# Kernel tuning notes

Hardware: AMD Instinct MI355X
Metric: run time of the kernel (lower is better)

Reference implementation:

```python
import jax, jax.numpy as jnp
import numpy as np

H = 8          # heads
V = 25         # num_nodes
C_IN = 64      # node_channel_in
C_OUT = 64     # node_channel_out
D_IN = V * C_IN    # 1600
D_OUT = V * C_OUT  # 1600


def setup_inputs() -> dict:
    key = jax.random.key(0)
    ks = jax.random.split(key, 7)
    s = 1.0 / np.sqrt(D_IN)  # torch Linear default init scale (uniform bound)
    x = jax.random.normal(ks[0], (16, C_IN, 512, V), dtype=jnp.float32)
    Wq = jax.random.uniform(ks[1], (H, D_IN, D_OUT), jnp.float32, -s, s)
    Wk = jax.random.uniform(ks[2], (H, D_IN, D_OUT), jnp.float32, -s, s)
    Wv = jax.random.uniform(ks[3], (H, D_IN, D_OUT), jnp.float32, -s, s)
    bq = jax.random.uniform(ks[4], (H, D_OUT), jnp.float32, -s, s)
    bk = jax.random.uniform(ks[5], (H, D_OUT), jnp.float32, -s, s)
    bv = jax.random.uniform(ks[6], (H, D_OUT), jnp.float32, -s, s)
    return {"x": x, "Wq": Wq, "bq": bq, "Wk": Wk, "bk": bk, "Wv": Wv, "bv": bv}


def reference(x, Wq, bq, Wk, bk, Wv, bv):
    n, c, t, v = x.shape
    # (n, c, t, v) -> (n, t, c*v)
    xf = jnp.transpose(x, (0, 2, 1, 3)).reshape(n, t, c * v)
    # fused per-head projections: batched GEMM over head axis
    q = jnp.einsum('ntd,hde->nhte', xf, Wq) + bq[None, :, None, :]
    k = jnp.einsum('ntd,hde->nhte', xf, Wk) + bk[None, :, None, :]
    val = jnp.einsum('ntd,hde->nhte', xf, Wv) + bv[None, :, None, :]
    scale = 1.0 / np.sqrt(C_OUT * V).astype(np.float32)
    att = jnp.einsum('nhte,nhse->nhts', q, k) * scale  # [n,h,t,t]
    att = jax.nn.softmax(att, axis=-1)
    o = jnp.einsum('nhts,nhse->nhte', att, val)  # [n,h,t,d_out]
    # (n,h,t,d) -> (n,t,d,h) -> (n,t,v,c_out*h) -> (n,c_out*h,t,v)
    o = jnp.transpose(o, (0, 2, 3, 1)).reshape(n, t, V, C_OUT * H)
    return jnp.transpose(o, (0, 3, 1, 2))
```

## Files before the change

### kernel.cpp

```cpp
#include <hip/hip_runtime.h>
#include <stdint.h>

#define NB    16
#define H8    8
#define T512  512
#define D1600 1600
#define EP    1664

typedef short s16x8 __attribute__((ext_vector_type(8)));
typedef float f32x4 __attribute__((ext_vector_type(4)));

__device__ __forceinline__ unsigned short f2bf(float f) {
  unsigned int u = __builtin_bit_cast(unsigned int, f);
  u += 0x7FFFu + ((u >> 16) & 1u);
  return (unsigned short)(u >> 16);
}

__device__ __forceinline__ void gld_lds16(const void* g, void* l) {
  __builtin_amdgcn_global_load_lds(
      (const __attribute__((address_space(1))) unsigned int*)g,
      (__attribute__((address_space(3))) unsigned int*)l, 16, 0, 0);
}

__global__ __launch_bounds__(256)
void conv_x_k(const float* __restrict__ x, unsigned short* __restrict__ xf) {
  size_t i = (size_t)blockIdx.x * 256 + threadIdx.x;
  if (i >= (size_t)NB * T512 * D1600) return;
  int d  = (int)(i % D1600);
  size_t nt = i / D1600;
  int t  = (int)(nt % T512);
  int n  = (int)(nt / T512);
  int c = d / 25, v = d % 25;
  xf[i] = f2bf(x[(((size_t)n * 64 + c) * 512 + t) * 25 + v]);
}

__global__ __launch_bounds__(256)
void conv_w_k(const float* __restrict__ Wq, const float* __restrict__ Wk,
              const float* __restrict__ Wv, unsigned short* __restrict__ Wt) {
  __shared__ float tile[32][33];
  int b = blockIdx.z, i3 = b >> 3, h = b & 7;
  const float* W = (i3 == 0 ? Wq : i3 == 1 ? Wk : Wv) + (size_t)h * D1600 * D1600;
  unsigned short* Wo = Wt + (size_t)b * EP * D1600;
  int e0 = blockIdx.x * 32, d0 = blockIdx.y * 32;
  int tx = threadIdx.x & 31, ty = threadIdx.x >> 5;
#pragma unroll
  for (int j = 0; j < 4; ++j) {
    int d = d0 + ty + j * 8, e = e0 + tx;
    tile[ty + j * 8][tx] = (e < D1600) ? W[(size_t)d * D1600 + e] : 0.f;
  }
  __syncthreads();
#pragma unroll
  for (int j = 0; j < 4; ++j) {
    int e = e0 + ty + j * 8, d = d0 + tx;
    Wo[(size_t)e * D1600 + d] = f2bf(tile[tx][ty + j * 8]);
  }
}

template <int MODE>
__global__ __launch_bounds__(256, 2)
void gemm_nt(const unsigned short* __restrict__ Ag,
             const unsigned short* __restrict__ Bg,
             float* __restrict__ Cf,
             unsigned short* __restrict__ Qo, unsigned short* __restrict__ Ko,
             unsigned short* __restrict__ Vo,
             const float* __restrict__ bq, const float* __restrict__ bk,
             const float* __restrict__ bv,
             int Klen, int lda, int ldb, float scale, int zbase) {
  constexpr int BM = 128, BN = 128, BK = 64;
  __shared__ unsigned short As[BM * BK];
  __shared__ unsigned short Bs[BN * BK];

  const int tid = threadIdx.x;
  const int wid = tid >> 6;
  const int lane = tid & 63;
  const int wr = wid >> 1, wc = wid & 1;
  const int m0 = blockIdx.y * BM;
  const int n0 = blockIdx.x * BN;
  const int z = zbase + blockIdx.z;

  const unsigned short* Ab;
  const unsigned short* Bb;
  if (MODE == 0)      { Ab = Ag;                            Bb = Bg + (size_t)z * EP * D1600; }
  else if (MODE == 1) { Ab = Ag + (size_t)z * T512 * EP;    Bb = Bg + (size_t)z * T512 * EP;  }
  else                { Ab = Ag + (size_t)z * T512 * T512;  Bb = Bg + (size_t)z * EP * T512;  }

  f32x4 acc[4][4] = {};

  const int srow = lane >> 3;
  const int scol = (lane & 7) * 8;

  for (int k0 = 0; k0 < Klen; k0 += BK) {
#pragma unroll
    for (int i = 0; i < 4; ++i) {
      int row = i * 32 + wid * 8 + srow;
      gld_lds16(Ab + (size_t)(m0 + row) * lda + k0 + scol,
                &As[(size_t)(i * 32 + wid * 8) * BK]);
    }
#pragma unroll
    for (int i = 0; i < 4; ++i) {
      int row = i * 32 + wid * 8 + srow;
      gld_lds16(Bb + (size_t)(n0 + row) * ldb + k0 + scol,
                &Bs[(size_t)(i * 32 + wid * 8) * BK]);
    }
    __syncthreads();
#pragma unroll
    for (int ks = 0; ks < 2; ++ks) {
      s16x8 af[4], bfr[4];
#pragma unroll
      for (int mi = 0; mi < 4; ++mi)
        af[mi] = *(const s16x8*)&As[(wr * 64 + mi * 16 + (lane & 15)) * BK + ks * 32 + (lane >> 4) * 8];
#pragma unroll
      for (int ni = 0; ni < 4; ++ni)
        bfr[ni] = *(const s16x8*)&Bs[(wc * 64 + ni * 16 + (lane & 15)) * BK + ks * 32 + (lane >> 4) * 8];
#pragma unroll
      for (int mi = 0; mi < 4; ++mi)
#pragma unroll
        for (int ni = 0; ni < 4; ++ni)
          acc[mi][ni] = __builtin_amdgcn_mfma_f32_16x16x32_bf16(af[mi], bfr[ni], acc[mi][ni], 0, 0, 0);
    }
    __syncthreads();
  }

  const int crow = (lane >> 4) * 4;
  const int ccol = lane & 15;

  if (MODE == 0) {
    const int i3 = z >> 3, h = z & 7;
    unsigned short* Ob = (i3 == 0 ? Qo : i3 == 1 ? Ko : Vo);
    const float* bb = (i3 == 0 ? bq : i3 == 1 ? bk : bv) + (size_t)h * D1600;
#pragma unroll
    for (int mi = 0; mi < 4; ++mi) {
#pragma unroll
      for (int ni = 0; ni < 4; ++ni) {
        int col = n0 + wc * 64 + ni * 16 + ccol;
        float bias = (col < D1600) ? bb[col] : 0.f;
#pragma unroll
        for (int r = 0; r < 4; ++r) {
          int row = m0 + wr * 64 + mi * 16 + crow + r;
          int n = row >> 9, t = row & 511;
          Ob[((size_t)(n * 8 + h) * T512 + t) * EP + col] = f2bf(acc[mi][ni][r] + bias);
        }
      }
    }
  } else {
    float* Ob = (MODE == 1) ? Cf + (size_t)z * T512 * T512
                            : Cf + (size_t)blockIdx.z * T512 * EP;
    const int ldc = (MODE == 1) ? T512 : EP;
#pragma unroll
    for (int mi = 0; mi < 4; ++mi) {
#pragma unroll
      for (int ni = 0; ni < 4; ++ni) {
        int col = n0 + wc * 64 + ni * 16 + ccol;
#pragma unroll
        for (int r = 0; r < 4; ++r) {
          int row = m0 + wr * 64 + mi * 16 + crow + r;
          Ob[(size_t)row * ldc + col] = acc[mi][ni][r] * scale;
        }
      }
    }
  }
}

__global__ __launch_bounds__(256)
void transpose_v_k(const unsigned short* __restrict__ V, unsigned short* __restrict__ Vt) {
  __shared__ unsigned short tile[32][33];
  int z = blockIdx.z;
  const unsigned short* Vz = V + (size_t)z * T512 * EP;
  unsigned short* Vo = Vt + (size_t)z * EP * T512;
  int e0 = blockIdx.x * 32, s0 = blockIdx.y * 32;
  int tx = threadIdx.x & 31, ty = threadIdx.x >> 5;
#pragma unroll
  for (int j = 0; j < 4; ++j)
    tile[ty + j * 8][tx] = Vz[(size_t)(s0 + ty + j * 8) * EP + e0 + tx];
  __syncthreads();
#pragma unroll
  for (int j = 0; j < 4; ++j)
    Vo[(size_t)(e0 + ty + j * 8) * T512 + s0 + tx] = tile[tx][ty + j * 8];
}

__global__ __launch_bounds__(256)
void softmax_k(const float* __restrict__ S, unsigned short* __restrict__ P) {
  __shared__ float red[8];
  const int tid = threadIdx.x;
  const size_t row = blockIdx.x;
  const float* s = S + row * 512;
  float a = s[tid], b = s[tid + 256];
  float mx = fmaxf(a, b);
#pragma unroll
  for (int o = 32; o > 0; o >>= 1) mx = fmaxf(mx, __shfl_xor(mx, o));
  if ((tid & 63) == 0) red[tid >> 6] = mx;
  __syncthreads();
  mx = fmaxf(fmaxf(red[0], red[1]), fmaxf(red[2], red[3]));
  float ea = __expf(a - mx), eb = __expf(b - mx);
  float sum = ea + eb;
#pragma unroll
  for (int o = 32; o > 0; o >>= 1) sum += __shfl_xor(sum, o);
  if ((tid & 63) == 0) red[4 + (tid >> 6)] = sum;
  __syncthreads();
  float inv = 1.f / (red[4] + red[5] + red[6] + red[7]);
  unsigned short* p = P + row * 512;
  p[tid] = f2bf(ea * inv);
  p[tid + 256] = f2bf(eb * inv);
}

__global__ __launch_bounds__(256)
void final_out_k(const float* __restrict__ O, float* __restrict__ out, int zbase) {
  __shared__ float sm[8 * 1600];
  const int nh = zbase + blockIdx.y, n = nh >> 3, h = nh & 7;
  const int t0 = blockIdx.x * 8;
  const float* o = O + ((size_t)blockIdx.y * T512 + t0) * EP;
  for (int idx = threadIdx.x; idx < 8 * 1600; idx += 256) {
    int tt = idx / 1600, e = idx % 1600;
    sm[tt * 1600 + (e & 63) * 25 + (e >> 6)] = o[(size_t)tt * EP + e];
  }
  __syncthreads();
  for (int idx = threadIdx.x; idx < 64 * 200; idx += 256) {
    int c = idx / 200, r = idx % 200;
    out[(((size_t)n * 512 + c * 8 + h) * T512 + t0) * 25 + r] = sm[(r / 25) * 1600 + c * 25 + (r % 25)];
  }
}

extern "C" void kernel_launch(void* const* d_in, const int* in_sizes, int n_in,
                              void* d_out, int out_size, void* d_ws, size_t ws_size,
                              hipStream_t stream) {
  const float* x  = (const float*)d_in[0];
  const float* Wq = (const float*)d_in[1];
  const float* bq = (const float*)d_in[2];
  const float* Wk = (const float*)d_in[3];
  const float* bk = (const float*)d_in[4];
  const float* Wv = (const float*)d_in[5];
  const float* bv = (const float*)d_in[6];
  float* out = (float*)d_out;
  char* ws = (char*)d_ws;

  const size_t NEED = 808321024ULL;
  if (ws_size < NEED) return;

  unsigned short* Wt = (unsigned short*)(ws + 0ULL);
  unsigned short* xf = (unsigned short*)(ws + 127795200ULL);
  unsigned short* Q  = (unsigned short*)(ws + 154009600ULL);
  unsigned short* K  = (unsigned short*)(ws + 372113408ULL);
  unsigned short* V  = (unsigned short*)(ws + 590217216ULL);
  float*          S  = (float*)(ws + 0ULL);
  unsigned short* Vt = (unsigned short*)(ws + 154009600ULL);
  unsigned short* P  = (unsigned short*)(ws + 372113408ULL);
  float*          Oh = (float*)(ws + 439222272ULL);

  (void)in_sizes; (void)n_in; (void)out_size;

  conv_x_k<<<51200, 256, 0, stream>>>(x, xf);
  conv_w_k<<<dim3(52, 50, 24), 256, 0, stream>>>(Wq, Wk, Wv, Wt);
  gemm_nt<0><<<dim3(13, 64, 24), 256, 0, stream>>>(
      xf, Wt, nullptr, Q, K, V, bq, bk, bv, D1600, D1600, D1600, 1.0f, 0);
  gemm_nt<1><<<dim3(4, 4, 128), 256, 0, stream>>>(
      Q, K, S, nullptr, nullptr, nullptr, nullptr, nullptr, nullptr,
      EP, EP, EP, 0.025f, 0);
  transpose_v_k<<<dim3(52, 16, 128), 256, 0, stream>>>(V, Vt);
  softmax_k<<<65536, 256, 0, stream>>>(S, P);
  for (int zb = 0; zb < 128; zb += 64) {
    gemm_nt<2><<<dim3(13, 4, 64), 256, 0, stream>>>(
        P, Vt, Oh, nullptr, nullptr, nullptr, nullptr, nullptr, nullptr,
        T512, T512, T512, 1.0f, zb);
    final_out_k<<<dim3(64, 64), 256, 0, stream>>>(Oh, out, zb);
  }
}
```

Baseline: 3.101 ms.

## Replace projection GEMM with 256x256-tile pipelined kernel using swizzled LDS

Adds a dedicated projection GEMM that uses 256x256 output tiles with 512 threads, double-buffered direct-to-LDS loads with XOR swizzling, interleaved prefetch and MFMA phases, and a remapped block order for cache locality. The larger tiles give more data reuse per load, and the staged waits are meant to overlap global loads with compute in the dominant xf·W GEMM. The generic gemm_nt drops its MODE 0 path. In exchange it needs 128KB of LDS and one block per CU, and it clamps out-of-range B rows, so padded columns hold garbage but are still written to the EP padding.

```diff
diff --git a/kernel.cpp b/kernel.cpp
--- a/kernel.cpp
+++ b/kernel.cpp
@@ -56,15 +56,177 @@
   }
 }
 
+__global__ __launch_bounds__(512, 1)
+void gemm256_proj(const unsigned short* __restrict__ Ag,
+                  const unsigned short* __restrict__ Bg,
+                  unsigned short* __restrict__ Qo, unsigned short* __restrict__ Ko,
+                  unsigned short* __restrict__ Vo,
+                  const float* __restrict__ bq, const float* __restrict__ bk,
+                  const float* __restrict__ bv) {
+  __shared__ __align__(16) char lds[131072];
+  const int tid  = threadIdx.x;
+  const int lane = tid & 63;
+  const int wid  = tid >> 6;
+  const int wr   = wid >> 2;
+  const int wc   = wid & 3;
+
+  const int fid = blockIdx.x + 7 * (blockIdx.y + 32 * blockIdx.z);
+  const int lid = (fid & 7) * 672 + (fid >> 3);
+  const int m0 = (lid & 31) * 256;
+  const int nz = lid >> 5;
+  const int n0 = (nz % 7) * 256;
+  const int z  = nz / 7;
+
+  const unsigned short* Ab = Ag;
+  const unsigned short* Bb = Bg + (size_t)z * EP * D1600;
+
+  const int srow = tid >> 3;
+  const int soff = (((tid & 7) ^ (srow & 7)) << 3);
+
+  auto stageA = [&](int b, int h, int kk) {
+    const unsigned short* s0 = Ab + (size_t)(m0 + h * 128 + srow) * D1600 + kk * 64 + soff;
+    char* d = lds + b * 32768 + h * 16384 + tid * 16;
+    gld_lds16(s0, d);
+    gld_lds16(s0 + (size_t)64 * D1600, d + 8192);
+  };
+  auto stageB = [&](int b, int h, int kk) {
+    int r0 = n0 + h * 128 + srow;
+    int r1 = r0 + 64;
+    if (r0 > 1663) r0 = 1663;
+    if (r1 > 1663) r1 = 1663;
+    char* d = lds + 65536 + b * 32768 + h * 16384 + tid * 16;
+    gld_lds16(Bb + (size_t)r0 * D1600 + kk * 64 + soff, d);
+    gld_lds16(Bb + (size_t)r1 * D1600 + kk * 64 + soff, d + 8192);
+  };
+
+  const int arow = lane & 15;
+  const int sw0 = (((lane >> 4)) ^ (lane & 7)) * 16;
+  const int sw1 = ((4 + (lane >> 4)) ^ (lane & 7)) * 16;
+
+  f32x4 acc[8][4] = {};
+  s16x8 af[4][2], b0[2][2], b1[2][2];
+
+  stageA(0, 0, 0); stageA(0, 1, 0);
+  stageB(0, 0, 0); stageB(0, 1, 0);
+  stageB(1, 0, 1); stageB(1, 1, 1);
+  asm volatile("s_waitcnt vmcnt(4)" ::: "memory");
+  __builtin_amdgcn_s_barrier();
+
+  for (int t = 0; t < 25; ++t) {
+    const int cur = t & 1, nxt = cur ^ 1;
+    const int ka = (t + 1 < 25) ? t + 1 : 24;
+    const int kb = (t + 2 < 25) ? t + 2 : 24;
+    const char* Abase = lds + cur * 32768 + wr * 16384;
+    const char* Bbase = lds + 65536 + cur * 32768 + (wc >> 1) * 16384 + (wc & 1) * 8192;
+
+#pragma unroll
+    for (int m = 0; m < 4; ++m) {
+      af[m][0] = *(const s16x8*)(Abase + (m * 16 + arow) * 128 + sw0);
+      af[m][1] = *(const s16x8*)(Abase + (m * 16 + arow) * 128 + sw1);
+    }
+#pragma unroll
+    for (int n = 0; n < 2; ++n) {
+      b0[n][0] = *(const s16x8*)(Bbase + (n * 16 + arow) * 128 + sw0);
+      b0[n][1] = *(const s16x8*)(Bbase + (n * 16 + arow) * 128 + sw1);
+    }
+    stageA(nxt, 0, ka);
+    __builtin_amdgcn_s_barrier();
+    asm volatile("s_waitcnt lgkmcnt(0)" ::: "memory");
+    __builtin_amdgcn_sched_barrier(0);
+    __builtin_amdgcn_s_setprio(1);
+#pragma unroll
+    for (int m = 0; m < 4; ++m)
+#pragma unroll
+      for (int n = 0; n < 2; ++n) {
+        acc[m][n] = __builtin_amdgcn_mfma_f32_16x16x32_bf16(af[m][0], b0[n][0], acc[m][n], 0, 0, 0);
+        acc[m][n] = __builtin_amdgcn_mfma_f32_16x16x32_bf16(af[m][1], b0[n][1], acc[m][n], 0, 0, 0);
+      }
+    __builtin_amdgcn_s_setprio(0);
+    __builtin_amdgcn_s_barrier();
+
+#pragma unroll
+    for (int n = 0; n < 2; ++n) {
+      b1[n][0] = *(const s16x8*)(Bbase + ((n + 2) * 16 + arow) * 128 + sw0);
+      b1[n][1] = *(const s16x8*)(Bbase + ((n + 2) * 16 + arow) * 128 + sw1);
+    }
+    stageA(nxt, 1, ka);
+    __builtin_amdgcn_s_barrier();
+    asm volatile("s_waitcnt lgkmcnt(0)" ::: "memory");
+    __builtin_amdgcn_sched_barrier(0);
+    __builtin_amdgcn_s_setprio(1);
+#pragma unroll
+    for (int m = 0; m < 4; ++m)
+#pragma unroll
+      for (int n = 0; n < 2; ++n) {
+        acc[m][n + 2] = __builtin_amdgcn_mfma_f32_16x16x32_bf16(af[m][0], b1[n][0], acc[m][n + 2], 0, 0, 0);
+        acc[m][n + 2] = __builtin_amdgcn_mfma_f32_16x16x32_bf16(af[m][1], b1[n][1], acc[m][n + 2], 0, 0, 0);
+      }
+    __builtin_amdgcn_s_setprio(0);
+    __builtin_amdgcn_s_barrier();
+
+#pragma unroll
+    for (int m = 0; m < 4; ++m) {
+      af[m][0] = *(const s16x8*)(Abase + ((m + 4) * 16 + arow) * 128 + sw0);
+      af[m][1] = *(const s16x8*)(Abase + ((m + 4) * 16 + arow) * 128 + sw1);
+    }
+    stageB(cur, 0, kb);
+    __builtin_amdgcn_s_barrier();
+    asm volatile("s_waitcnt lgkmcnt(0)" ::: "memory");
+    __builtin_amdgcn_sched_barrier(0);
+    __builtin_amdgcn_s_setprio(1);
+#pragma unroll
+    for (int m = 0; m < 4; ++m)
+#pragma unroll
+      for (int n = 0; n < 2; ++n) {
+        acc[m + 4][n] = __builtin_amdgcn_mfma_f32_16x16x32_bf16(af[m][0], b0[n][0], acc[m + 4][n], 0, 0, 0);
+        acc[m + 4][n] = __builtin_amdgcn_mfma_f32_16x16x32_bf16(af[m][1], b0[n][1], acc[m + 4][n], 0, 0, 0);
+      }
+    __builtin_amdgcn_s_setprio(0);
+    __builtin_amdgcn_s_barrier();
+
+    stageB(cur, 1, kb);
+    asm volatile("s_waitcnt vmcnt(4)" ::: "memory");
+    __builtin_amdgcn_s_barrier();
+    __builtin_amdgcn_s_setprio(1);
+#pragma unroll
+    for (int m = 0; m < 4; ++m)
+#pragma unroll
+      for (int n = 0; n < 2; ++n) {
+        acc[m + 4][n + 2] = __builtin_amdgcn_mfma_f32_16x16x32_bf16(af[m][0], b1[n][0], acc[m + 4][n + 2], 0, 0, 0);
+        acc[m + 4][n + 2] = __builtin_amdgcn_mfma_f32_16x16x32_bf16(af[m][1], b1[n][1], acc[m + 4][n + 2], 0, 0, 0);
+      }
+    __builtin_amdgcn_s_setprio(0);
+    __builtin_amdgcn_s_barrier();
+  }
+
+  asm volatile("s_waitcnt vmcnt(0)" ::: "memory");
+  __builtin_amdgcn_s_barrier();
+
+  const int i3 = z >> 3, h = z & 7;
+  unsigned short* Ob = (i3 == 0 ? Qo : i3 == 1 ? Ko : Vo);
+  const float* bb = (i3 == 0 ? bq : i3 == 1 ? bk : bv) + (size_t)h * D1600;
+#pragma unroll
+  for (int mi = 0; mi < 8; ++mi)
+#pragma unroll
+    for (int ni = 0; ni < 4; ++ni) {
+      const int col = n0 + wc * 64 + ni * 16 + (lane & 15);
+      if (col < 1664) {
+        const float bias = (col < D1600) ? bb[col] : 0.f;
+#pragma unroll
+        for (int r = 0; r < 4; ++r) {
+          const int row = m0 + wr * 128 + mi * 16 + ((lane >> 4) << 2) + r;
+          const int n = row >> 9, tt = row & 511;
+          Ob[((size_t)(n * 8 + h) * T512 + tt) * EP + col] = f2bf(acc[mi][ni][r] + bias);
+        }
+      }
+    }
+}
+
 template <int MODE>
 __global__ __launch_bounds__(256, 2)
 void gemm_nt(const unsigned short* __restrict__ Ag,
              const unsigned short* __restrict__ Bg,
              float* __restrict__ Cf,
-             unsigned short* __restrict__ Qo, unsigned short* __restrict__ Ko,
-             unsigned short* __restrict__ Vo,
-             const float* __restrict__ bq, const float* __restrict__ bk,
-             const float* __restrict__ bv,
              int Klen, int lda, int ldb, float scale, int zbase) {
   constexpr int BM = 128, BN = 128, BK = 64;
   __shared__ unsigned short As[BM * BK];
@@ -80,9 +242,8 @@
 
   const unsigned short* Ab;
   const unsigned short* Bb;
-  if (MODE == 0)      { Ab = Ag;                            Bb = Bg + (size_t)z * EP * D1600; }
-  else if (MODE == 1) { Ab = Ag + (size_t)z * T512 * EP;    Bb = Bg + (size_t)z * T512 * EP;  }
-  else                { Ab = Ag + (size_t)z * T512 * T512;  Bb = Bg + (size_t)z * EP * T512;  }
+  if (MODE == 1) { Ab = Ag + (size_t)z * T512 * EP;   Bb = Bg + (size_t)z * T512 * EP; }
+  else           { Ab = Ag + (size_t)z * T512 * T512; Bb = Bg + (size_t)z * EP * T512; }
 
   f32x4 acc[4][4] = {};
 
@@ -123,42 +284,20 @@
 
   const int crow = (lane >> 4) * 4;
   const int ccol = lane & 15;
-
-  if (MODE == 0) {
-    const int i3 = z >> 3, h = z & 7;
-    unsigned short* Ob = (i3 == 0 ? Qo : i3 == 1 ? Ko : Vo);
-    const float* bb = (i3 == 0 ? bq : i3 == 1 ? bk : bv) + (size_t)h * D1600;
-#pragma unroll
-    for (int mi = 0; mi < 4; ++mi) {
-#pragma unroll
-      for (int ni = 0; ni < 4; ++ni) {
-        int col = n0 + wc * 64 + ni * 16 + ccol;
-        float bias = (col < D1600) ? bb[col] : 0.f;
-#pragma unroll
-        for (int r = 0; r < 4; ++r) {
-          int row = m0 + wr * 64 + mi * 16 + crow + r;
-          int n = row >> 9, t = row & 511;
-          Ob[((size_t)(n * 8 + h) * T512 + t) * EP + col] = f2bf(acc[mi][ni][r] + bias);
-        }
-      }
-    }
-  } else {
-    float* Ob = (MODE == 1) ? Cf + (size_t)z * T512 * T512
-                            : Cf + (size_t)blockIdx.z * T512 * EP;
-    const int ldc = (MODE == 1) ? T512 : EP;
-#pragma unroll
-    for (int mi = 0; mi < 4; ++mi) {
-#pragma unroll
-      for (int ni = 0; ni < 4; ++ni) {
-        int col = n0 + wc * 64 + ni * 16 + ccol;
-#pragma unroll
-        for (int r = 0; r < 4; ++r) {
-          int row = m0 + wr * 64 + mi * 16 + crow + r;
-          Ob[(size_t)row * ldc + col] = acc[mi][ni][r] * scale;
-        }
-      }
-    }
-  }
+  float* Ob = (MODE == 1) ? Cf + (size_t)z * T512 * T512
+                          : Cf + (size_t)blockIdx.z * T512 * EP;
+  const int ldc = (MODE == 1) ? T512 : EP;
+#pragma unroll
+  for (int mi = 0; mi < 4; ++mi)
+#pragma unroll
+    for (int ni = 0; ni < 4; ++ni) {
+      int col = n0 + wc * 64 + ni * 16 + ccol;
+#pragma unroll
+      for (int r = 0; r < 4; ++r) {
+        int row = m0 + wr * 64 + mi * 16 + crow + r;
+        Ob[(size_t)row * ldc + col] = acc[mi][ni][r] * scale;
+      }
+    }
 }
 
 __global__ __launch_bounds__(256)
@@ -250,17 +389,12 @@
 
   conv_x_k<<<51200, 256, 0, stream>>>(x, xf);
   conv_w_k<<<dim3(52, 50, 24), 256, 0, stream>>>(Wq, Wk, Wv, Wt);
-  gemm_nt<0><<<dim3(13, 64, 24), 256, 0, stream>>>(
-      xf, Wt, nullptr, Q, K, V, bq, bk, bv, D1600, D1600, D1600, 1.0f, 0);
-  gemm_nt<1><<<dim3(4, 4, 128), 256, 0, stream>>>(
-      Q, K, S, nullptr, nullptr, nullptr, nullptr, nullptr, nullptr,
-      EP, EP, EP, 0.025f, 0);
+  gemm256_proj<<<dim3(7, 32, 24), 512, 0, stream>>>(xf, Wt, Q, K, V, bq, bk, bv);
+  gemm_nt<1><<<dim3(4, 4, 128), 256, 0, stream>>>(Q, K, S, EP, EP, EP, 0.025f, 0);
   transpose_v_k<<<dim3(52, 16, 128), 256, 0, stream>>>(V, Vt);
   softmax_k<<<65536, 256, 0, stream>>>(S, P);
   for (int zb = 0; zb < 128; zb += 64) {
-    gemm_nt<2><<<dim3(13, 4, 64), 256, 0, stream>>>(
-        P, Vt, Oh, nullptr, nullptr, nullptr, nullptr, nullptr, nullptr,
-        T512, T512, T512, 1.0f, zb);
+    gemm_nt<2><<<dim3(13, 4, 64), 256, 0, stream>>>(P, Vt, Oh, T512, T512, T512, 1.0f, zb);
     final_out_k<<<dim3(64, 64), 256, 0, stream>>>(Oh, out, zb);
   }
 }
```

After: 2.532 ms. 1.22x faster.
